# Optimization experiments

Measured on AMD Instinct MI355X. Metric: run time of the kernel, lower is better.

## Reference

```python
import jax, jax.numpy as jnp
import numpy as np

B, P, K, KS = 512, 64, 30, 4      # graphs, nodes per graph, sort-pool k, conv1d kernel
N, E, F, H = B * P, 524288, 128, 256
N_CLASSES = 10
L_OUT = K - KS + 1                 # 27, conv1d output length


def _sage(h, wl, wr, b, src, dst, inv_deg):
    # PyG SAGEConv (mean aggr): out = lin_l(mean_j x_j) + lin_r(x_i); bias only on lin_l
    agg = jax.ops.segment_sum(h[src], dst, num_segments=N) * inv_deg
    return jax.nn.relu(agg @ wl + b + h @ wr)


def setup_inputs() -> dict:
    key = jax.random.key(0)
    ks = jax.random.split(key, 32)
    x = jax.random.normal(ks[0], (N, F), jnp.float32)
    # intra-graph random edges (src -> dst aggregation)
    g = jax.random.randint(ks[1], (E,), 0, B)
    src = g * P + jax.random.randint(ks[2], (E,), 0, P)
    dst = g * P + jax.random.randint(ks[3], (E,), 0, P)
    edge_index = jnp.stack([src, dst]).astype(jnp.int32)
    batch = jnp.repeat(jnp.arange(B), P).astype(jnp.int32)  # sorted graph ids

    def lin(k, i, o):
        return jax.random.normal(k, (i, o), jnp.float32) / np.float32(np.sqrt(i))

    inp = {"x": x, "edge_index": edge_index, "batch": batch}
    dims = [(F, H), (H, H), (H, H), (H, H)]
    ki = 4
    for li, (i, o) in enumerate(dims):
        inp[f"sage{li}_wl"] = lin(ks[ki], i, o); ki += 1
        inp[f"sage{li}_wr"] = lin(ks[ki], i, o); ki += 1
        inp[f"sage{li}_b"] = jnp.zeros((o,), jnp.float32)
    inp["conv1d_w"] = jax.random.normal(ks[ki], (H, H, KS), jnp.float32) / np.float32(np.sqrt(H * KS)); ki += 1
    inp["conv1d_b"] = jnp.zeros((H,), jnp.float32)
    inp["lin1_w"] = lin(ks[ki], H * L_OUT, H); ki += 1
    inp["lin1_b"] = jnp.zeros((H,), jnp.float32)
    inp["lin2_w"] = lin(ks[ki], H, 128); ki += 1
    inp["lin2_b"] = jnp.zeros((128,), jnp.float32)
    inp["out_w"] = lin(ks[ki], 128, N_CLASSES); ki += 1
    inp["out_b"] = jnp.zeros((N_CLASSES,), jnp.float32)
    return inp


def reference(x, edge_index, batch,
              sage0_wl, sage0_wr, sage0_b,
              sage1_wl, sage1_wr, sage1_b,
              sage2_wl, sage2_wr, sage2_b,
              sage3_wl, sage3_wr, sage3_b,
              conv1d_w, conv1d_b, lin1_w, lin1_b,
              lin2_w, lin2_b, out_w, out_b):
    src, dst = edge_index[0], edge_index[1]
    deg = jax.ops.segment_sum(jnp.ones(src.shape, x.dtype), dst, num_segments=N)
    inv_deg = (1.0 / jnp.maximum(deg, 1.0))[:, None]

    h = jnp.nan_to_num(x, nan=0.0)
    h = _sage(h, sage0_wl, sage0_wr, sage0_b, src, dst, inv_deg)
    h = _sage(h, sage1_wl, sage1_wr, sage1_b, src, dst, inv_deg)
    h = _sage(h, sage2_wl, sage2_wr, sage2_b, src, dst, inv_deg)
    h = _sage(h, sage3_wl, sage3_wr, sage3_b, src, dst, inv_deg)  # [N, H]

    # SortAggregation(k=K): to dense batch, sort by last channel desc, top-k, zero-pad
    counts = jax.ops.segment_sum(jnp.ones(N, jnp.int32), batch, num_segments=B)
    offsets = jnp.cumsum(counts) - counts
    pos = jnp.arange(N) - offsets[batch]
    D = h.shape[1]
    dense = jnp.zeros((B, P, D), h.dtype).at[batch, pos].set(h)
    valid = jnp.zeros((B, P), bool).at[batch, pos].set(True)
    skey = jnp.where(valid, dense[..., -1], -jnp.inf)
    order = jnp.argsort(-skey, axis=1)[:, :K]                       # [B, K]
    topk = jnp.take_along_axis(dense, order[..., None], axis=1)     # [B, K, D]
    tvalid = jnp.take_along_axis(valid, order, axis=1)
    topk = jnp.where(tvalid[..., None], topk, 0.0)

    # x.view(B, K, -1).permute(0, 2, 1) -> [B, D, K]
    xc = topk.transpose(0, 2, 1)
    y = jax.lax.conv_general_dilated(xc, conv1d_w, (1,), 'VALID',
                                     dimension_numbers=('NCH', 'OIH', 'NCH'))
    y = jax.nn.relu(y + conv1d_b[None, :, None])                    # [B, H, L_OUT]
    y = y.reshape(B, -1)                                            # dropout is identity in eval
    y = jax.nn.relu(y @ lin1_w + lin1_b)
    y = jax.nn.relu(y @ lin2_w + lin2_b)
    return jax.nn.relu(y @ out_w + out_b)                           # [B, N_CLASSES]
```

## Files before the change

### kernel.cpp

```cpp
#include <hip/hip_runtime.h>
#include <hip/hip_bf16.h>

#define NNODES 32768
#define NEDGES 524288
#define NGRAPH 512
#define PNODES 64
#define KTOP 30
#define FIN 128
#define HID 256
#define LOUT 27

#define C1F 4.8828125e-4f
#define C2F 2.384185791015625e-7f

using f16x8 = __attribute__((ext_vector_type(8))) _Float16;
using f16x4 = __attribute__((ext_vector_type(4))) _Float16;
using f32x4 = __attribute__((ext_vector_type(4))) float;
using f32x16 = __attribute__((ext_vector_type(16))) float;

#define GLDS(src, dst) __builtin_amdgcn_global_load_lds( \
    (const __attribute__((address_space(1))) void*)(src), \
    (__attribute__((address_space(3))) void*)(dst), 16, 0, 0)

__global__ void hist_kernel(const int* __restrict__ dst, int* __restrict__ counts) {
    int e = blockIdx.x * blockDim.x + threadIdx.x;
    if (e < NEDGES) atomicAdd(&counts[dst[e]], 1);
}

__global__ __launch_bounds__(1024) void scan_block_kernel(const int* __restrict__ counts,
        int* __restrict__ loc, int* __restrict__ partial) {
    int b = blockIdx.x, t = threadIdx.x;
    int i = b * 1024 + t;
    int v = counts[i];
    int lane = t & 63, w = t >> 6;
    int x = v;
    #pragma unroll
    for (int d = 1; d < 64; d <<= 1) { int y = __shfl_up(x, d, 64); if (lane >= d) x += y; }
    __shared__ int ws[16];
    if (lane == 63) ws[w] = x;
    __syncthreads();
    if (w == 0) {
        int s = (lane < 16) ? ws[lane] : 0;
        #pragma unroll
        for (int d = 1; d < 16; d <<= 1) { int y = __shfl_up(s, d, 64); if (lane >= d) s += y; }
        if (lane < 16) ws[lane] = s;
    }
    __syncthreads();
    int base = (w > 0) ? ws[w - 1] : 0;
    int incl = base + x;
    loc[i] = incl - v;
    if (t == 1023) partial[b] = incl;
}

__global__ __launch_bounds__(1024) void scan_fixup_kernel(const int* __restrict__ loc,
        const int* __restrict__ partial, const int* __restrict__ counts,
        int* __restrict__ offsets, int* __restrict__ cursor, float* __restrict__ invdeg) {
    int b = blockIdx.x, t = threadIdx.x;
    int i = b * 1024 + t;
    __shared__ int sbase;
    if (t == 0) { int s = 0; for (int j = 0; j < b; ++j) s += partial[j]; sbase = s; }
    __syncthreads();
    int o = loc[i] + sbase;
    offsets[i] = o;
    cursor[i] = o;
    invdeg[i] = 1.0f / fmaxf((float)counts[i], 1.0f);
}

__global__ void scatter_kernel(const int* __restrict__ src, const int* __restrict__ dst,
        int* __restrict__ cursor, int* __restrict__ ssrc) {
    int e = blockIdx.x * blockDim.x + threadIdx.x;
    if (e < NEDGES) {
        int d = dst[e];
        int p = atomicAdd(&cursor[d], 1);
        ssrc[p] = src[e];
    }
}

__global__ void nan2num_split_kernel(const float* __restrict__ x,
        _Float16* __restrict__ oh, _Float16* __restrict__ ol, int n4) {
    int i = blockIdx.x * blockDim.x + threadIdx.x;
    if (i >= n4) return;
    float4 v = *(const float4*)(x + i * 4);
    float xs[4] = {v.x, v.y, v.z, v.w};
    f16x4 hh, ll;
    #pragma unroll
    for (int q = 0; q < 4; ++q) {
        float a = xs[q];
        a = (a != a) ? 0.f : a;
        _Float16 h = (_Float16)a;
        hh[q] = h;
        ll[q] = (_Float16)((a - (float)h) * 2048.0f);
    }
    *(f16x4*)(oh + (size_t)i * 4) = hh;
    *(f16x4*)(ol + (size_t)i * 4) = ll;
}

struct Prep8 {
    const float* src[8];
    _Float16* dh[8];
    _Float16* dl[8];
    int logK[8];
    int nelem[8];
};

__global__ __launch_bounds__(256) void prep8_kernel(Prep8 p) {
    int y = blockIdx.y;
    int idx = blockIdx.x * 256 + threadIdx.x;
    if (idx >= p.nelem[y]) return;
    int lk = p.logK[y], K = 1 << lk;
    int n = idx >> lk, k = idx & (K - 1);
    float w = p.src[y][(size_t)k * 256 + n];
    _Float16 h = (_Float16)w;
    p.dh[y][(size_t)n * K + k] = h;
    p.dl[y][(size_t)n * K + k] = (_Float16)((w - (float)h) * 2048.0f);
}

__global__ __launch_bounds__(256) void prep_conv_kernel(const float* __restrict__ W,
        _Float16* __restrict__ b0, _Float16* __restrict__ b1) {
    int idx = blockIdx.x * 256 + threadIdx.x;
    int o = idx >> 10, k = idx & 1023;
    float w = W[(size_t)o * 1024 + (k & 255) * 4 + (k >> 8)];
    _Float16 h = (_Float16)w;
    b0[(size_t)o * 1024 + k] = h;
    b1[(size_t)o * 1024 + k] = (_Float16)((w - (float)h) * 2048.0f);
}

__global__ __launch_bounds__(256) void prep_lin1_kernel(const float* __restrict__ l1w,
        _Float16* __restrict__ wh, _Float16* __restrict__ wl_) {
    __shared__ float sh[64][65];
    int kb = blockIdx.x * 64;
    int nb = blockIdx.y * 64;
    int t = threadIdx.x;
    {
        int kk = t >> 2;
        int nc = (t & 3) * 16;
        int k = kb + kk, l = k >> 8, c = k & 255;
        const float* srow = l1w + (size_t)(c * 27 + l) * 256 + nb + nc;
        #pragma unroll
        for (int j = 0; j < 16; j += 4) {
            float4 v = *(const float4*)(srow + j);
            sh[kk][nc + j + 0] = v.x;
            sh[kk][nc + j + 1] = v.y;
            sh[kk][nc + j + 2] = v.z;
            sh[kk][nc + j + 3] = v.w;
        }
    }
    __syncthreads();
    {
        int nn = t >> 2;
        int kc = (t & 3) * 16;
        f16x8 oh[2], ol[2];
        #pragma unroll
        for (int j = 0; j < 16; ++j) {
            float x = sh[kc + j][nn];
            _Float16 h = (_Float16)x;
            oh[j >> 3][j & 7] = h;
            ol[j >> 3][j & 7] = (_Float16)((x - (float)h) * 2048.0f);
        }
        size_t o = (size_t)(nb + nn) * 6912 + kb + kc;
        *(f16x8*)(wh + o) = oh[0];
        *(f16x8*)(wh + o + 8) = oh[1];
        *(f16x8*)(wl_ + o) = ol[0];
        *(f16x8*)(wl_ + o + 8) = ol[1];
    }
}

template<int H, int LOGH>
__global__ __launch_bounds__(256) void aggregate_ps_kernel(
        const _Float16* __restrict__ hh, const _Float16* __restrict__ hl,
        const int* __restrict__ offsets, const int* __restrict__ counts,
        const int* __restrict__ ssrc, const float* __restrict__ invdeg,
        _Float16* __restrict__ aggh, _Float16* __restrict__ aggl) {
    __shared__ float sh[64 * H];
    const int g = blockIdx.x, t = threadIdx.x;
    const size_t base = (size_t)g * 64 * H;
    for (int i4 = t * 4; i4 < 64 * H; i4 += 1024) {
        f16x4 vh = *(const f16x4*)(hh + base + i4);
        f16x4 vl = *(const f16x4*)(hl + base + i4);
        int row = i4 >> LOGH, col = i4 & (H - 1);
        int sw = row & 28;
        float4 v = make_float4(
            (float)vh[0] + C1F * (float)vl[0],
            (float)vh[1] + C1F * (float)vl[1],
            (float)vh[2] + C1F * (float)vl[2],
            (float)vh[3] + C1F * (float)vl[3]);
        *(float4*)&sh[(row << LOGH) + (col ^ sw)] = v;
    }
    __syncthreads();
    const int n = t >> 2, fb = t & 3;
    const int FQ = H >> 2;
    const int node = g * 64 + n;
    const int beg = offsets[node], cnt = counts[node];
    float acc[FQ];
    #pragma unroll
    for (int j = 0; j < FQ; ++j) acc[j] = 0.f;
    for (int e = 0; e < cnt; ++e) {
        int sn = ssrc[beg + e] & 63;
        int rowoff = sn << LOGH;
        int sw = sn & 28;
        #pragma unroll
        for (int j = 0; j < FQ; j += 4) {
            int f = fb * FQ + (j ^ (fb * 8));
            float4 v = *(float4*)&sh[rowoff + (f ^ sw)];
            acc[j]     += v.x;
            acc[j + 1] += v.y;
            acc[j + 2] += v.z;
            acc[j + 3] += v.w;
        }
    }
    float s = invdeg[node];
    __syncthreads();
    {
        int rowoff = n << LOGH;
        int sw = n & 28;
        #pragma unroll
        for (int j = 0; j < FQ; j += 4) {
            int f = fb * FQ + (j ^ (fb * 8));
            *(float4*)&sh[rowoff + (f ^ sw)] =
                make_float4(acc[j] * s, acc[j + 1] * s, acc[j + 2] * s, acc[j + 3] * s);
        }
    }
    __syncthreads();
    for (int i4 = t * 4; i4 < 64 * H; i4 += 1024) {
        int row = i4 >> LOGH, col = i4 & (H - 1);
        int sw = row & 28;
        float4 v = *(float4*)&sh[(row << LOGH) + (col ^ sw)];
        float xs[4] = {v.x, v.y, v.z, v.w};
        f16x4 oh, ol;
        #pragma unroll
        for (int q = 0; q < 4; ++q) {
            _Float16 h = (_Float16)xs[q];
            oh[q] = h;
            ol[q] = (_Float16)((xs[q] - (float)h) * 2048.0f);
        }
        *(f16x4*)(aggh + base + i4) = oh;
        *(f16x4*)(aggl + base + i4) = ol;
    }
}

template<int NPROD, int CONV, int NPAIRS, int EPI>
__global__ __launch_bounds__(256, 2) void mfma_ps_kernel(
        const _Float16* __restrict__ A1h, const _Float16* __restrict__ A1l,
        const _Float16* __restrict__ A2h, const _Float16* __restrict__ A2l,
        const _Float16* __restrict__ B1h, const _Float16* __restrict__ B1l,
        const _Float16* __restrict__ B2h, const _Float16* __restrict__ B2l,
        const float* __restrict__ bias,
        _Float16* __restrict__ outh, _Float16* __restrict__ outl,
        float* __restrict__ Cpart,
        int lda, int K, int Nd, int nrb) {
    __shared__ _Float16 As[2][2][128 * 32];
    __shared__ _Float16 Bs[2][2][128 * 32];
    const int t = threadIdx.x;
    const int lane = t & 63, wave = t >> 6;
    const int wr = wave & 1, wc = wave >> 1;
    const int bid = blockIdx.x;
    const int rb = bid % nrb, cb = bid / nrb;
    const int row0 = rb * 128, col0 = cb * 128;
    const int l31 = lane & 31, hb = lane >> 5, x3 = l31 & 3;
    const int r16 = lane >> 2;
    const int qsrc8 = ((lane & 3) ^ (r16 & 3)) * 8;
    size_t aoffj[2], boffj[2];
    #pragma unroll
    for (int j = 0; j < 2; ++j) {
        int ar = row0 + wave * 32 + j * 16 + r16;
        aoffj[j] = CONV ? ((size_t)ar * 256 + (size_t)(ar / 27) * 768)
                        : (size_t)ar * (size_t)lda;
        boffj[j] = (size_t)(col0 + wave * 32 + j * 16 + r16) * (size_t)K;
    }
    int aroff[2], broff[2], slot8[2];
    #pragma unroll
    for (int mi = 0; mi < 2; ++mi) aroff[mi] = (wr * 64 + mi * 32 + l31) * 32;
    #pragma unroll
    for (int ni = 0; ni < 2; ++ni) broff[ni] = (wc * 64 + ni * 32 + l31) * 32;
    #pragma unroll
    for (int h = 0; h < 2; ++h) slot8[h] = ((2 * h + hb) ^ x3) * 8;

    const int KV = NPAIRS * K;
    const int kchunk = KV / gridDim.z;
    const int kv_lo = blockIdx.z * kchunk, kv_hi = kv_lo + kchunk;

    f32x16 acc0[2][2], acc1[2][2], acc2[2][2];
    #pragma unroll
    for (int i = 0; i < 2; ++i)
        #pragma unroll
        for (int j = 0; j < 2; ++j) { acc0[i][j] = 0.f; acc1[i][j] = 0.f; acc2[i][j] = 0.f; }

    auto stage = [&](int kv, int b) {
        int p = (NPAIRS == 2 && kv >= K) ? 1 : 0;
        int k = kv - p * K;
        const _Float16* __restrict__ sAh = p ? A2h : A1h;
        const _Float16* __restrict__ sAl = p ? A2l : A1l;
        const _Float16* __restrict__ sBh = p ? B2h : B1h;
        const _Float16* __restrict__ sBl = p ? B2l : B1l;
        #pragma unroll
        for (int j = 0; j < 2; ++j) {
            int ldsbase = (wave * 32 + j * 16) * 32;
            size_t ga = aoffj[j] + k + qsrc8;
            size_t gb = boffj[j] + k + qsrc8;
            GLDS(sAh + ga, &As[b][0][ldsbase]);
            GLDS(sAl + ga, &As[b][1][ldsbase]);
            GLDS(sBh + gb, &Bs[b][0][ldsbase]);
            GLDS(sBl + gb, &Bs[b][1][ldsbase]);
        }
    };

    stage(kv_lo, 0);
    __syncthreads();
    int b = 0;
    for (int kv = kv_lo; kv < kv_hi; kv += 32) {
        if (kv + 32 < kv_hi) stage(kv + 32, b ^ 1);
        #pragma unroll
        for (int h = 0; h < 2; ++h) {
            f16x8 af0[2], af1[2], bf0[2], bf1[2];
            #pragma unroll
            for (int mi = 0; mi < 2; ++mi) {
                af0[mi] = *(const f16x8*)&As[b][0][aroff[mi] + slot8[h]];
                af1[mi] = *(const f16x8*)&As[b][1][aroff[mi] + slot8[h]];
            }
            #pragma unroll
            for (int ni = 0; ni < 2; ++ni) {
                bf0[ni] = *(const f16x8*)&Bs[b][0][broff[ni] + slot8[h]];
                bf1[ni] = *(const f16x8*)&Bs[b][1][broff[ni] + slot8[h]];
            }
            #pragma unroll
            for (int mi = 0; mi < 2; ++mi)
                #pragma unroll
                for (int ni = 0; ni < 2; ++ni) {
                    acc0[mi][ni] = __builtin_amdgcn_mfma_f32_32x32x16_f16(af0[mi], bf0[ni], acc0[mi][ni], 0, 0, 0);
                    acc1[mi][ni] = __builtin_amdgcn_mfma_f32_32x32x16_f16(af1[mi], bf0[ni], acc1[mi][ni], 0, 0, 0);
                    acc1[mi][ni] = __builtin_amdgcn_mfma_f32_32x32x16_f16(af0[mi], bf1[ni], acc1[mi][ni], 0, 0, 0);
                    if (NPROD == 4)
                        acc2[mi][ni] = __builtin_amdgcn_mfma_f32_32x32x16_f16(af1[mi], bf1[ni], acc2[mi][ni], 0, 0, 0);
                }
        }
        b ^= 1;
        __syncthreads();
    }

    const int rquad = 4 * hb;
    #pragma unroll
    for (int ni = 0; ni < 2; ++ni) {
        int col = col0 + wc * 64 + ni * 32 + l31;
        float bb = (EPI == 0) ? bias[col] : 0.f;
        #pragma unroll
        for (int mi = 0; mi < 2; ++mi) {
            #pragma unroll
            for (int reg = 0; reg < 16; ++reg) {
                float v = acc0[mi][ni][reg] + C1F * acc1[mi][ni][reg];
                if (NPROD == 4) v += C2F * acc2[mi][ni][reg];
                int row = row0 + wr * 64 + mi * 32 + (reg & 3) + 8 * (reg >> 2) + rquad;
                if (EPI == 0) {
                    v = fmaxf(v + bb, 0.f);
                    _Float16 h = (_Float16)v;
                    size_t o = (size_t)row * Nd + col;
                    outh[o] = h;
                    outl[o] = (_Float16)((v - (float)h) * 2048.0f);
                } else {
                    size_t zb = (size_t)blockIdx.z * (size_t)(nrb * 128) * Nd;
                    Cpart[zb + (size_t)row * Nd + col] = v;
                }
            }
        }
    }
}

__global__ __launch_bounds__(256) void sortgather_kernel(const _Float16* __restrict__ hh,
        const _Float16* __restrict__ hl, _Float16* __restrict__ th, _Float16* __restrict__ tl) {
    __shared__ float vals[PNODES];
    __shared__ int ord[KTOP];
    int g = blockIdx.x, t = threadIdx.x;
    if (t < PNODES) {
        size_t idx = (size_t)(g * PNODES + t) * HID + (HID - 1);
        vals[t] = (float)hh[idx] + C1F * (float)hl[idx];
    }
    __syncthreads();
    if (t < PNODES) {
        float v = vals[t];
        int rank = 0;
        for (int j = 0; j < PNODES; ++j) {
            float vj = vals[j];
            rank += (vj > v) || (vj == v && j < t);
        }
        if (rank < KTOP) ord[rank] = g * PNODES + t;
    }
    __syncthreads();
    for (int r = 0; r < KTOP; ++r) {
        size_t s = (size_t)ord[r] * HID + t;
        size_t d = (size_t)(g * KTOP + r) * HID + t;
        th[d] = hh[s];
        tl[d] = hl[s];
    }
}

__global__ void reduce_conv_kernel(const float* __restrict__ yb32,
        const float* __restrict__ b, _Float16* __restrict__ ybh, _Float16* __restrict__ ybl) {
    int i = blockIdx.x * 256 + threadIdx.x;
    float v = fmaxf(yb32[i] + yb32[i + 13824 * 256] + b[i & 255], 0.f);
    _Float16 h = (_Float16)v;
    ybh[i] = h;
    ybl[i] = (_Float16)((v - (float)h) * 2048.0f);
}

__global__ void reduce_lin1_kernel(const float* __restrict__ z1p,
        const float* __restrict__ b, float* __restrict__ z1) {
    int i = blockIdx.x * 256 + threadIdx.x;
    float s = b[i & 255];
    #pragma unroll
    for (int z = 0; z < 27; ++z) s += z1p[(size_t)z * 131072 + i];
    z1[i] = fmaxf(s, 0.f);
}

__global__ __launch_bounds__(256) void gemm64_kernel(
        const float* __restrict__ A, const float* __restrict__ B,
        const float* __restrict__ bias, float* __restrict__ C,
        int lda, int kend, int Nd) {
    __shared__ float As[16][64];
    __shared__ float Bs[16][64];
    const int tid = threadIdx.x;
    const int tx = tid & 15, ty = tid >> 4;
    const int la_r = tid >> 2, la_c = (tid & 3) << 2;
    const int lb_r = tid >> 4, lb_c = (tid & 15) << 2;
    const int row0 = blockIdx.x * 64, col0 = blockIdx.y * 64;
    const size_t aoff = (size_t)(row0 + la_r) * (size_t)lda;
    float acc[4][4] = {};
    for (int k0 = 0; k0 < kend; k0 += 16) {
        __syncthreads();
        float4 av = *(const float4*)(A + aoff + k0 + la_c);
        As[la_c + 0][la_r] = av.x;
        As[la_c + 1][la_r] = av.y;
        As[la_c + 2][la_r] = av.z;
        As[la_c + 3][la_r] = av.w;
        *(float4*)&Bs[lb_r][lb_c] = *(const float4*)(B + (size_t)(k0 + lb_r) * Nd + col0 + lb_c);
        __syncthreads();
        #pragma unroll
        for (int k = 0; k < 16; ++k) {
            float4 a = *(const float4*)&As[k][ty << 2];
            float4 b = *(const float4*)&Bs[k][tx << 2];
            acc[0][0] += a.x * b.x; acc[0][1] += a.x * b.y; acc[0][2] += a.x * b.z; acc[0][3] += a.x * b.w;
            acc[1][0] += a.y * b.x; acc[1][1] += a.y * b.y; acc[1][2] += a.y * b.z; acc[1][3] += a.y * b.w;
            acc[2][0] += a.z * b.x; acc[2][1] += a.z * b.y; acc[2][2] += a.z * b.z; acc[2][3] += a.z * b.w;
            acc[3][0] += a.w * b.x; acc[3][1] += a.w * b.y; acc[3][2] += a.w * b.z; acc[3][3] += a.w * b.w;
        }
    }
    #pragma unroll
    for (int i = 0; i < 4; ++i) {
        int row = row0 + (ty << 2) + i;
        #pragma unroll
        for (int j = 0; j < 4; ++j) {
            int col = col0 + (tx << 2) + j;
            C[(size_t)row * Nd + col] = fmaxf(acc[i][j] + bias[col], 0.f);
        }
    }
}

__global__ void out_kernel(const float* __restrict__ z2, const float* __restrict__ w,
        const float* __restrict__ b, float* __restrict__ out) {
    int idx = blockIdx.x * blockDim.x + threadIdx.x;
    if (idx < NGRAPH * 10) {
        int r = idx / 10, c = idx % 10;
        float s = b[c];
        for (int k = 0; k < 128; ++k) s += z2[r * 128 + k] * w[k * 10 + c];
        out[idx] = fmaxf(s, 0.f);
    }
}

extern "C" void kernel_launch(void* const* d_in, const int* in_sizes, int n_in,
                              void* d_out, int out_size, void* d_ws, size_t ws_size,
                              hipStream_t stream) {
    const float* x    = (const float*)d_in[0];
    const int*   edge = (const int*)d_in[1];
    const int*   esrc = edge;
    const int*   edst = edge + NEDGES;
    const float* wl[4] = {(const float*)d_in[3], (const float*)d_in[6], (const float*)d_in[9],  (const float*)d_in[12]};
    const float* wr[4] = {(const float*)d_in[4], (const float*)d_in[7], (const float*)d_in[10], (const float*)d_in[13]};
    const float* sb[4] = {(const float*)d_in[5], (const float*)d_in[8], (const float*)d_in[11], (const float*)d_in[14]};
    const float* convw = (const float*)d_in[15];
    const float* convb = (const float*)d_in[16];
    const float* l1w   = (const float*)d_in[17];
    const float* l1b   = (const float*)d_in[18];
    const float* l2w   = (const float*)d_in[19];
    const float* l2b   = (const float*)d_in[20];
    const float* ow    = (const float*)d_in[21];
    const float* ob    = (const float*)d_in[22];
    float* out = (float*)d_out;

    char* ws = (char*)d_ws;
    size_t off = 0;
    auto alloc = [&](size_t bytes) -> char* {
        char* p = ws + off;
        off = (off + bytes + 255) & ~(size_t)255;
        return p;
    };
    int*   counts  = (int*)alloc((size_t)NNODES * 4);
    int*   offsets = (int*)alloc((size_t)NNODES * 4);
    int*   cursor  = (int*)alloc((size_t)NNODES * 4);
    int*   loc     = (int*)alloc((size_t)NNODES * 4);
    int*   partial = (int*)alloc(32 * 4);
    float* invdeg  = (float*)alloc((size_t)NNODES * 4);
    int*   ssrc    = (int*)alloc((size_t)NEDGES * 4);
    _Float16* wlh[4]; _Float16* wll[4]; _Float16* wrh[4]; _Float16* wrl[4];
    for (int l = 0; l < 4; ++l) {
        size_t kb = (size_t)(l ? HID : FIN) * HID * 2;
        wlh[l] = (_Float16*)alloc(kb); wll[l] = (_Float16*)alloc(kb);
        wrh[l] = (_Float16*)alloc(kb); wrl[l] = (_Float16*)alloc(kb);
    }
    _Float16* cvh = (_Float16*)alloc((size_t)HID * 1024 * 2);
    _Float16* cvl = (_Float16*)alloc((size_t)HID * 1024 * 2);

    const size_t H0T = (size_t)NNODES * FIN * 2;
    const size_t AGT = (size_t)NNODES * HID * 2;
    const size_t TKT = (size_t)NGRAPH * KTOP * HID * 2;
    const size_t YBT = (size_t)NGRAPH * LOUT * HID * 2;
    const size_t YB32T = (size_t)2 * 13824 * 256 * 4;
    const size_t Z1PT = (size_t)27 * NGRAPH * HID * 4;
    const size_t W1T = (size_t)HID * 6912 * 2;

    char* R1 = alloc(2 * H0T);
    char* R2 = alloc(2 * AGT);
    char* R3 = alloc(2 * AGT);
    char* R4 = alloc(2 * AGT);
    _Float16* h0h = (_Float16*)R1; _Float16* h0l = (_Float16*)(R1 + H0T);
    _Float16* tkh = (_Float16*)R1; _Float16* tkl = (_Float16*)(R1 + TKT);
    _Float16* aggh = (_Float16*)R2; _Float16* aggl = (_Float16*)(R2 + AGT);
    _Float16* hAh = (_Float16*)R3; _Float16* hAl = (_Float16*)(R3 + AGT);
    _Float16* ybh = (_Float16*)R2; _Float16* ybl_ = (_Float16*)(R2 + YBT);
    float* yb32 = (float*)(R2 + 2 * YBT);
    float* z1p  = (float*)(R2 + 2 * YBT);
    char* tail2 = R2 + 2 * YBT + YB32T;
    float* z1  = (float*)tail2;
    float* z2  = (float*)(tail2 + (size_t)NGRAPH * HID * 4);
    _Float16* w1h = (_Float16*)(tail2 + (size_t)NGRAPH * HID * 4 + (size_t)NGRAPH * 128 * 4 + 256);
    _Float16* w1l = (_Float16*)((char*)w1h + W1T);
    _Float16* hBh = (_Float16*)R4; _Float16* hBl = (_Float16*)(R4 + AGT);

    hipMemsetAsync(counts, 0, (size_t)NNODES * 4, stream);
    hist_kernel<<<NEDGES / 256, 256, 0, stream>>>(edst, counts);
    scan_block_kernel<<<NNODES / 1024, 1024, 0, stream>>>(counts, loc, partial);
    scan_fixup_kernel<<<NNODES / 1024, 1024, 0, stream>>>(loc, partial, counts, offsets, cursor, invdeg);
    scatter_kernel<<<NEDGES / 256, 256, 0, stream>>>(esrc, edst, cursor, ssrc);
    nan2num_split_kernel<<<(NNODES * FIN / 4) / 256, 256, 0, stream>>>(x, h0h, h0l, NNODES * FIN / 4);

    Prep8 p8;
    for (int l = 0; l < 4; ++l) {
        int K = l ? HID : FIN, lk = l ? 8 : 7;
        p8.src[2 * l] = wl[l];     p8.dh[2 * l] = wlh[l];     p8.dl[2 * l] = wll[l];
        p8.src[2 * l + 1] = wr[l]; p8.dh[2 * l + 1] = wrh[l]; p8.dl[2 * l + 1] = wrl[l];
        p8.logK[2 * l] = lk;   p8.nelem[2 * l] = 256 * K;
        p8.logK[2 * l + 1] = lk; p8.nelem[2 * l + 1] = 256 * K;
    }
    prep8_kernel<<<dim3(256, 8), 256, 0, stream>>>(p8);
    prep_conv_kernel<<<(HID * 1024) / 256, 256, 0, stream>>>(convw, cvh, cvl);

    aggregate_ps_kernel<FIN, 7><<<NGRAPH, 256, 0, stream>>>(h0h, h0l, offsets, counts, ssrc, invdeg, aggh, aggl);
    mfma_ps_kernel<3, 0, 2, 0><<<dim3(256 * 2, 1, 1), 256, 0, stream>>>(
        aggh, aggl, h0h, h0l, wlh[0], wll[0], wrh[0], wrl[0], sb[0], hAh, hAl, nullptr, FIN, FIN, HID, 256);
    _Float16* hinh = hAh; _Float16* hinl = hAl;
    _Float16* hoth = hBh; _Float16* hotl = hBl;
    for (int l = 1; l < 4; ++l) {
        aggregate_ps_kernel<HID, 8><<<NGRAPH, 256, 0, stream>>>(hinh, hinl, offsets, counts, ssrc, invdeg, aggh, aggl);
        mfma_ps_kernel<3, 0, 2, 0><<<dim3(256 * 2, 1, 1), 256, 0, stream>>>(
            aggh, aggl, hinh, hinl, wlh[l], wll[l], wrh[l], wrl[l], sb[l], hoth, hotl, nullptr, HID, HID, HID, 256);
        _Float16* t1 = hinh; hinh = hoth; hoth = t1;
        _Float16* t2 = hinl; hinl = hotl; hotl = t2;
    }

    sortgather_kernel<<<NGRAPH, 256, 0, stream>>>(hinh, hinl, tkh, tkl);
    prep_lin1_kernel<<<dim3(108, 4), 256, 0, stream>>>(l1w, w1h, w1l);

    mfma_ps_kernel<3, 1, 1, 1><<<dim3(108 * 2, 1, 2), 256, 0, stream>>>(
        tkh, tkl, nullptr, nullptr, cvh, cvl, nullptr, nullptr, nullptr, nullptr, nullptr, yb32, 256, 1024, HID, 108);
    reduce_conv_kernel<<<13824 * 256 / 256, 256, 0, stream>>>(yb32, convb, ybh, ybl_);

    mfma_ps_kernel<3, 0, 1, 1><<<dim3(4 * 2, 1, 27), 256, 0, stream>>>(
        ybh, ybl_, nullptr, nullptr, w1h, w1l, nullptr, nullptr, nullptr, nullptr, nullptr, z1p, 6912, 6912, HID, 4);
    reduce_lin1_kernel<<<NGRAPH * HID / 256, 256, 0, stream>>>(z1p, l1b, z1);

    gemm64_kernel<<<dim3(NGRAPH / 64, 128 / 64), 256, 0, stream>>>(z1, l2w, l2b, z2, HID, HID, 128);

    out_kernel<<<(NGRAPH * 10 + 255) / 256, 256, 0, stream>>>(z2, ow, ob, out);
}
```

Baseline: 492.0 us.

## Fuse SAGE neighbor aggregation and linear layers into one per-graph kernel

```diff
diff --git a/kernel.cpp b/kernel.cpp
--- a/kernel.cpp
+++ b/kernel.cpp
@@ -101,6 +101,7 @@
     _Float16* dl[8];
     int logK[8];
     int nelem[8];
+    int rstride[8];
 };
 
 __global__ __launch_bounds__(256) void prep8_kernel(Prep8 p) {
@@ -111,8 +112,8 @@
     int n = idx >> lk, k = idx & (K - 1);
     float w = p.src[y][(size_t)k * 256 + n];
     _Float16 h = (_Float16)w;
-    p.dh[y][(size_t)n * K + k] = h;
-    p.dl[y][(size_t)n * K + k] = (_Float16)((w - (float)h) * 2048.0f);
+    p.dh[y][(size_t)n * p.rstride[y] + k] = h;
+    p.dl[y][(size_t)n * p.rstride[y] + k] = (_Float16)((w - (float)h) * 2048.0f);
 }
 
 __global__ __launch_bounds__(256) void prep_conv_kernel(const float* __restrict__ W,
@@ -165,76 +166,157 @@
     }
 }
 
-template<int H, int LOGH>
-__global__ __launch_bounds__(256) void aggregate_ps_kernel(
+template<int HIN, int LOGHIN>
+__global__ __launch_bounds__(512, 2) void fused_sage_kernel(
         const _Float16* __restrict__ hh, const _Float16* __restrict__ hl,
         const int* __restrict__ offsets, const int* __restrict__ counts,
         const int* __restrict__ ssrc, const float* __restrict__ invdeg,
-        _Float16* __restrict__ aggh, _Float16* __restrict__ aggl) {
-    __shared__ float sh[64 * H];
+        const _Float16* __restrict__ Wh, const _Float16* __restrict__ Wl,
+        const float* __restrict__ bias,
+        _Float16* __restrict__ outh, _Float16* __restrict__ outl) {
+    constexpr int KV = 2 * HIN;
+    constexpr int NP = HIN / 32;
+    constexpr int TILE = 64 * HIN;
+    __shared__ __align__(16) float hsm[TILE];
+    __shared__ __align__(16) _Float16 am[2][TILE];
+    _Float16* hp0 = reinterpret_cast<_Float16*>(hsm);
+    _Float16* hp1 = hp0 + TILE;
     const int g = blockIdx.x, t = threadIdx.x;
-    const size_t base = (size_t)g * 64 * H;
-    for (int i4 = t * 4; i4 < 64 * H; i4 += 1024) {
+    const int lane = t & 63, wave = t >> 6;
+    const size_t base = (size_t)g * TILE;
+
+    for (int i4 = t * 4; i4 < TILE; i4 += 2048) {
         f16x4 vh = *(const f16x4*)(hh + base + i4);
         f16x4 vl = *(const f16x4*)(hl + base + i4);
-        int row = i4 >> LOGH, col = i4 & (H - 1);
+        int row = i4 >> LOGHIN, col = i4 & (HIN - 1);
         int sw = row & 28;
-        float4 v = make_float4(
+        *(float4*)&hsm[(row << LOGHIN) + (col ^ sw)] = make_float4(
             (float)vh[0] + C1F * (float)vl[0],
             (float)vh[1] + C1F * (float)vl[1],
             (float)vh[2] + C1F * (float)vl[2],
             (float)vh[3] + C1F * (float)vl[3]);
-        *(float4*)&sh[(row << LOGH) + (col ^ sw)] = v;
-    }
-    __syncthreads();
-    const int n = t >> 2, fb = t & 3;
-    const int FQ = H >> 2;
-    const int node = g * 64 + n;
-    const int beg = offsets[node], cnt = counts[node];
-    float acc[FQ];
-    #pragma unroll
-    for (int j = 0; j < FQ; ++j) acc[j] = 0.f;
+    }
+    __syncthreads();
+
+    const int node = t >> 3, q = t & 7;
+    const int gnode = g * 64 + node;
+    const int beg = offsets[gnode], cnt = counts[gnode];
+    const float s = invdeg[gnode];
+    float acc[NP][4];
+    #pragma unroll
+    for (int p = 0; p < NP; ++p) { acc[p][0] = 0.f; acc[p][1] = 0.f; acc[p][2] = 0.f; acc[p][3] = 0.f; }
     for (int e = 0; e < cnt; ++e) {
         int sn = ssrc[beg + e] & 63;
-        int rowoff = sn << LOGH;
-        int sw = sn & 28;
-        #pragma unroll
-        for (int j = 0; j < FQ; j += 4) {
-            int f = fb * FQ + (j ^ (fb * 8));
-            float4 v = *(float4*)&sh[rowoff + (f ^ sw)];
-            acc[j]     += v.x;
-            acc[j + 1] += v.y;
-            acc[j + 2] += v.z;
-            acc[j + 3] += v.w;
-        }
-    }
-    float s = invdeg[node];
-    __syncthreads();
+        int ro = sn << LOGHIN, sw = sn & 28;
+        #pragma unroll
+        for (int p = 0; p < NP; ++p) {
+            int f = p * 32 + q * 4;
+            float4 v = *(const float4*)&hsm[ro + (f ^ sw)];
+            acc[p][0] += v.x; acc[p][1] += v.y; acc[p][2] += v.z; acc[p][3] += v.w;
+        }
+    }
+    float hv[NP][4];
     {
-        int rowoff = n << LOGH;
-        int sw = n & 28;
-        #pragma unroll
-        for (int j = 0; j < FQ; j += 4) {
-            int f = fb * FQ + (j ^ (fb * 8));
-            *(float4*)&sh[rowoff + (f ^ sw)] =
-                make_float4(acc[j] * s, acc[j + 1] * s, acc[j + 2] * s, acc[j + 3] * s);
-        }
-    }
-    __syncthreads();
-    for (int i4 = t * 4; i4 < 64 * H; i4 += 1024) {
-        int row = i4 >> LOGH, col = i4 & (H - 1);
-        int sw = row & 28;
-        float4 v = *(float4*)&sh[(row << LOGH) + (col ^ sw)];
-        float xs[4] = {v.x, v.y, v.z, v.w};
-        f16x4 oh, ol;
-        #pragma unroll
-        for (int q = 0; q < 4; ++q) {
-            _Float16 h = (_Float16)xs[q];
-            oh[q] = h;
-            ol[q] = (_Float16)((xs[q] - (float)h) * 2048.0f);
-        }
-        *(f16x4*)(aggh + base + i4) = oh;
-        *(f16x4*)(aggl + base + i4) = ol;
+        int ro = node << LOGHIN, sw = node & 28;
+        #pragma unroll
+        for (int p = 0; p < NP; ++p) {
+            int f = p * 32 + q * 4;
+            float4 v = *(const float4*)&hsm[ro + (f ^ sw)];
+            hv[p][0] = v.x; hv[p][1] = v.y; hv[p][2] = v.z; hv[p][3] = v.w;
+        }
+    }
+    __syncthreads();
+
+    {
+        int slot = ((q >> 1) ^ (node & 3)) * 8 + (q & 1) * 4;
+        int a0 = node * 32 + slot;
+        #pragma unroll
+        for (int p = 0; p < NP; ++p) {
+            int addr = p * 2048 + a0;
+            f16x4 ah, al, bh4, bl4;
+            #pragma unroll
+            for (int j = 0; j < 4; ++j) {
+                float va = acc[p][j] * s;
+                _Float16 h1 = (_Float16)va;
+                ah[j] = h1; al[j] = (_Float16)((va - (float)h1) * 2048.0f);
+                float vb = hv[p][j];
+                _Float16 h2 = (_Float16)vb;
+                bh4[j] = h2; bl4[j] = (_Float16)((vb - (float)h2) * 2048.0f);
+            }
+            *(f16x4*)&am[0][addr] = ah;
+            *(f16x4*)&am[1][addr] = al;
+            *(f16x4*)&hp0[addr] = bh4;
+            *(f16x4*)&hp1[addr] = bl4;
+        }
+    }
+    __syncthreads();
+
+    const int l31 = lane & 31, hb = lane >> 5;
+    const int col = wave * 32 + l31;
+    const _Float16* __restrict__ Brh = Wh + (size_t)col * KV;
+    const _Float16* __restrict__ Brl = Wl + (size_t)col * KV;
+    f32x16 acc0[2], acc1[2];
+    #pragma unroll
+    for (int mi = 0; mi < 2; ++mi) { acc0[mi] = 0.f; acc1[mi] = 0.f; }
+
+    f16x8 a0f[2][2][2], a1f[2][2][2];
+    f16x8 bhf[2][2], blf[2][2];
+    constexpr int nC = KV / 32;
+
+    auto loadA = [&](int c, int buf) {
+        int kv = c * 32;
+        const _Float16* sh = (kv < HIN) ? &am[0][0] : hp0;
+        const _Float16* sl = (kv < HIN) ? &am[1][0] : hp1;
+        int pbase = ((kv & (HIN - 1)) >> 5) * 2048;
+        #pragma unroll
+        for (int h2 = 0; h2 < 2; ++h2)
+            #pragma unroll
+            for (int mi = 0; mi < 2; ++mi) {
+                int row = mi * 32 + l31;
+                int addr = pbase + row * 32 + (((2 * h2 + hb) ^ (row & 3)) * 8);
+                a0f[buf][h2][mi] = *(const f16x8*)&sh[addr];
+                a1f[buf][h2][mi] = *(const f16x8*)&sl[addr];
+            }
+    };
+    auto loadB = [&](int c, int buf) {
+        int kv = c * 32;
+        #pragma unroll
+        for (int h2 = 0; h2 < 2; ++h2) {
+            int o = kv + h2 * 16 + hb * 8;
+            bhf[buf][h2] = *(const f16x8*)(Brh + o);
+            blf[buf][h2] = *(const f16x8*)(Brl + o);
+        }
+    };
+
+    loadA(0, 0); loadB(0, 0);
+    #pragma unroll 2
+    for (int c = 0; c < nC; ++c) {
+        int cur = c & 1, nxt = cur ^ 1;
+        if (c + 1 < nC) { loadA(c + 1, nxt); loadB(c + 1, nxt); }
+        #pragma unroll
+        for (int h2 = 0; h2 < 2; ++h2)
+            #pragma unroll
+            for (int mi = 0; mi < 2; ++mi) {
+                acc0[mi] = __builtin_amdgcn_mfma_f32_32x32x16_f16(a0f[cur][h2][mi], bhf[cur][h2], acc0[mi], 0, 0, 0);
+                acc1[mi] = __builtin_amdgcn_mfma_f32_32x32x16_f16(a1f[cur][h2][mi], bhf[cur][h2], acc1[mi], 0, 0, 0);
+                acc1[mi] = __builtin_amdgcn_mfma_f32_32x32x16_f16(a0f[cur][h2][mi], blf[cur][h2], acc1[mi], 0, 0, 0);
+            }
+    }
+
+    const int rq = 4 * hb;
+    const float bb = bias[col];
+    #pragma unroll
+    for (int mi = 0; mi < 2; ++mi) {
+        #pragma unroll
+        for (int reg = 0; reg < 16; ++reg) {
+            float v = acc0[mi][reg] + C1F * acc1[mi][reg];
+            int row = mi * 32 + (reg & 3) + 8 * (reg >> 2) + rq;
+            v = fmaxf(v + bb, 0.f);
+            _Float16 h1 = (_Float16)v;
+            size_t o = (size_t)(g * 64 + row) * HID + col;
+            outh[o] = h1;
+            outl[o] = (_Float16)((v - (float)h1) * 2048.0f);
+        }
     }
 }
 
@@ -384,11 +466,12 @@
         if (rank < KTOP) ord[rank] = g * PNODES + t;
     }
     __syncthreads();
-    for (int r = 0; r < KTOP; ++r) {
-        size_t s = (size_t)ord[r] * HID + t;
-        size_t d = (size_t)(g * KTOP + r) * HID + t;
-        th[d] = hh[s];
-        tl[d] = hl[s];
+    int c8 = (t & 31) * 8;
+    for (int r = t >> 5; r < KTOP; r += 8) {
+        size_t s = (size_t)ord[r] * HID + c8;
+        size_t d = (size_t)(g * KTOP + r) * HID + c8;
+        *(f16x8*)(th + d) = *(const f16x8*)(hh + s);
+        *(f16x8*)(tl + d) = *(const f16x8*)(hl + s);
     }
 }
 
@@ -498,11 +581,11 @@
     int*   partial = (int*)alloc(32 * 4);
     float* invdeg  = (float*)alloc((size_t)NNODES * 4);
     int*   ssrc    = (int*)alloc((size_t)NEDGES * 4);
-    _Float16* wlh[4]; _Float16* wll[4]; _Float16* wrh[4]; _Float16* wrl[4];
+    _Float16* wch[4]; _Float16* wcl[4];
     for (int l = 0; l < 4; ++l) {
-        size_t kb = (size_t)(l ? HID : FIN) * HID * 2;
-        wlh[l] = (_Float16*)alloc(kb); wll[l] = (_Float16*)alloc(kb);
-        wrh[l] = (_Float16*)alloc(kb); wrl[l] = (_Float16*)alloc(kb);
+        size_t kb = (size_t)256 * 2 * (l ? HID : FIN) * 2;
+        wch[l] = (_Float16*)alloc(kb);
+        wcl[l] = (_Float16*)alloc(kb);
     }
     _Float16* cvh = (_Float16*)alloc((size_t)HID * 1024 * 2);
     _Float16* cvl = (_Float16*)alloc((size_t)HID * 1024 * 2);
@@ -521,7 +604,6 @@
     char* R4 = alloc(2 * AGT);
     _Float16* h0h = (_Float16*)R1; _Float16* h0l = (_Float16*)(R1 + H0T);
     _Float16* tkh = (_Float16*)R1; _Float16* tkl = (_Float16*)(R1 + TKT);
-    _Float16* aggh = (_Float16*)R2; _Float16* aggl = (_Float16*)(R2 + AGT);
     _Float16* hAh = (_Float16*)R3; _Float16* hAl = (_Float16*)(R3 + AGT);
     _Float16* ybh = (_Float16*)R2; _Float16* ybl_ = (_Float16*)(R2 + YBT);
     float* yb32 = (float*)(R2 + 2 * YBT);
@@ -543,23 +625,21 @@
     Prep8 p8;
     for (int l = 0; l < 4; ++l) {
         int K = l ? HID : FIN, lk = l ? 8 : 7;
-        p8.src[2 * l] = wl[l];     p8.dh[2 * l] = wlh[l];     p8.dl[2 * l] = wll[l];
-        p8.src[2 * l + 1] = wr[l]; p8.dh[2 * l + 1] = wrh[l]; p8.dl[2 * l + 1] = wrl[l];
-        p8.logK[2 * l] = lk;   p8.nelem[2 * l] = 256 * K;
-        p8.logK[2 * l + 1] = lk; p8.nelem[2 * l + 1] = 256 * K;
+        p8.src[2 * l] = wl[l];     p8.dh[2 * l] = wch[l];         p8.dl[2 * l] = wcl[l];
+        p8.src[2 * l + 1] = wr[l]; p8.dh[2 * l + 1] = wch[l] + K; p8.dl[2 * l + 1] = wcl[l] + K;
+        p8.logK[2 * l] = lk;     p8.nelem[2 * l] = 256 * K;     p8.rstride[2 * l] = 2 * K;
+        p8.logK[2 * l + 1] = lk; p8.nelem[2 * l + 1] = 256 * K; p8.rstride[2 * l + 1] = 2 * K;
     }
     prep8_kernel<<<dim3(256, 8), 256, 0, stream>>>(p8);
     prep_conv_kernel<<<(HID * 1024) / 256, 256, 0, stream>>>(convw, cvh, cvl);
 
-    aggregate_ps_kernel<FIN, 7><<<NGRAPH, 256, 0, stream>>>(h0h, h0l, offsets, counts, ssrc, invdeg, aggh, aggl);
-    mfma_ps_kernel<3, 0, 2, 0><<<dim3(256 * 2, 1, 1), 256, 0, stream>>>(
-        aggh, aggl, h0h, h0l, wlh[0], wll[0], wrh[0], wrl[0], sb[0], hAh, hAl, nullptr, FIN, FIN, HID, 256);
+    fused_sage_kernel<FIN, 7><<<NGRAPH, 512, 0, stream>>>(
+        h0h, h0l, offsets, counts, ssrc, invdeg, wch[0], wcl[0], sb[0], hAh, hAl);
     _Float16* hinh = hAh; _Float16* hinl = hAl;
     _Float16* hoth = hBh; _Float16* hotl = hBl;
     for (int l = 1; l < 4; ++l) {
-        aggregate_ps_kernel<HID, 8><<<NGRAPH, 256, 0, stream>>>(hinh, hinl, offsets, counts, ssrc, invdeg, aggh, aggl);
-        mfma_ps_kernel<3, 0, 2, 0><<<dim3(256 * 2, 1, 1), 256, 0, stream>>>(
-            aggh, aggl, hinh, hinl, wlh[l], wll[l], wrh[l], wrl[l], sb[l], hoth, hotl, nullptr, HID, HID, HID, 256);
+        fused_sage_kernel<HID, 8><<<NGRAPH, 512, 0, stream>>>(
+            hinh, hinl, offsets, counts, ssrc, invdeg, wch[l], wcl[l], sb[l], hoth, hotl);
         _Float16* t1 = hinh; hinh = hoth; hoth = t1;
         _Float16* t2 = hinl; hinl = hotl; hotl = t2;
     }
```

Measured after the change: 493.8 us. No clear change (+0.4%).
